# Performance work log

Measured on AMD Instinct MI355X. Metric: run time of the kernel, lower is better.

Reference implementation:

```python
import jax, jax.numpy as jnp
import numpy as np

N, IN_DIM, UNITS, Z_DEPTH, Z_K = 8192, 1024, 512, 32, 256


def setup_inputs() -> dict:
    key = jax.random.key(0)
    ks = jax.random.split(key, 10)
    s = 0.02
    return {
        "x": jax.random.normal(ks[0], (N, IN_DIM), jnp.float32),
        "h_W": jax.random.normal(ks[1], (IN_DIM, UNITS), jnp.float32) * s,
        "h_U": jax.random.normal(ks[2], (UNITS, UNITS), jnp.float32) * s,
        "h_b": jnp.zeros((UNITS,), jnp.float32),
        "f_W": jax.random.normal(ks[3], (UNITS, UNITS), jnp.float32) * s,
        "f_b": jnp.zeros((UNITS,), jnp.float32),
        "i_W": jax.random.normal(ks[4], (UNITS, UNITS), jnp.float32) * s,
        "i_b": jnp.zeros((UNITS,), jnp.float32),
        "c_W": jax.random.normal(ks[5], (UNITS, UNITS), jnp.float32) * s,
        "c_b": jnp.zeros((UNITS,), jnp.float32),
        "o_W": jax.random.normal(ks[6], (UNITS, UNITS), jnp.float32) * s,
        "o_b": jnp.zeros((UNITS,), jnp.float32),
        "t_W": jax.random.normal(ks[7], (UNITS, UNITS), jnp.float32) * s,
        "t_b": jnp.zeros((UNITS,), jnp.float32),
        "y_W": jax.random.normal(ks[8], (UNITS, Z_K), jnp.float32) * s,
        "y_b": jnp.zeros((Z_K,), jnp.float32),
        "h0": jnp.zeros((1, UNITS), jnp.float32),
        "z_depth": Z_DEPTH,
    }


def reference(x, h_W, h_U, h_b, f_W, f_b, i_W, i_b, c_W, c_b, o_W, o_b,
              t_W, t_b, y_W, y_b, h0, z_depth):
    n = x.shape[0]
    # x @ h_W is the same every step; hoist it out of the scan.
    xh = x @ h_W + h_b  # [n, units]

    def step(h_prev, _):
        h = jnp.tanh(xh + h_prev @ h_U)
        f = jax.nn.sigmoid(h @ f_W + f_b)
        i = jax.nn.sigmoid(h @ i_W + i_b)
        c = jnp.tanh(h @ c_W + c_b)
        o = jax.nn.sigmoid(h @ o_W + o_b)
        h1 = h_prev * f + c * i
        t = jnp.tanh((o * h1) @ t_W + t_b)
        y = jnp.tanh(t @ y_W + y_b)  # activation=tanh
        return h1, y

    h_init = jnp.broadcast_to(h0, (n, h0.shape[1]))
    _, ys = jax.lax.scan(step, h_init, None, length=z_depth)  # ys: [z_depth, n, z_k]
    return jnp.transpose(ys, (1, 0, 2))  # [n, z_depth, z_k]
```

## Files before the change

### kernel.cpp

```cpp
#include <hip/hip_runtime.h>


typedef _Float16 half_t;
typedef _Float16 half8 __attribute__((ext_vector_type(8)));
typedef _Float16 half4v __attribute__((ext_vector_type(4)));
typedef float float4_ __attribute__((ext_vector_type(4)));

#define UNITS 512
#define IN_DIM 1024
#define NROWS 8192
#define DEPTH 32
#define ZK 256
#define MT 64
#define PITCH (UNITS + 8)
#define XPITCH (IN_DIM + 8)

__device__ inline float4_ mfma16(half8 a, half8 b, float4_ c) {
  return __builtin_amdgcn_mfma_f32_16x16x32_f16(a, b, c, 0, 0, 0);
}
__device__ inline float fast_sigmoid(float x) {
  return __builtin_amdgcn_rcpf(1.0f + __builtin_amdgcn_exp2f(-1.4426950408889634f * x));
}
__device__ inline float fast_tanh(float x) {
  return 2.0f * __builtin_amdgcn_rcpf(1.0f + __builtin_amdgcn_exp2f(-2.8853900817779268f * x)) - 1.0f;
}

template<int NM, class OffF>
__device__ inline void sweepW(const half_t* __restrict__ wbase, OffF off,
                              const half_t* __restrict__ abase,
                              float4_ (&acc)[NM][4]) {
#pragma unroll
  for (int i = 0; i < NM; ++i)
#pragma unroll
    for (int rb = 0; rb < 4; ++rb) acc[i][rb] = {0.f, 0.f, 0.f, 0.f};
  for (int k0 = 0; k0 < UNITS; k0 += 64) {
    half8 a0[4], a1[4];
#pragma unroll
    for (int rb = 0; rb < 4; ++rb) {
      a0[rb] = *(const half8*)(abase + rb * 16 * PITCH + k0);
      a1[rb] = *(const half8*)(abase + rb * 16 * PITCH + k0 + 32);
    }
#pragma unroll
    for (int i = 0; i < NM; ++i) {
      const half_t* wp = wbase + off(i) + k0;
      half8 w0 = *(const half8*)(wp);
      half8 w1 = *(const half8*)(wp + 32);
#pragma unroll
      for (int rb = 0; rb < 4; ++rb) {
        acc[i][rb] = mfma16(w0, a0[rb], acc[i][rb]);
        acc[i][rb] = mfma16(w1, a1[rb], acc[i][rb]);
      }
    }
  }
}

template<int NB, int K, int AP, class OffF>
__device__ inline void stage_gemm(const half_t* __restrict__ bbase, OffF off,
                                  const half_t* __restrict__ A, int q, int c16,
                                  float4_ (&acc)[NB][2]) {
#pragma unroll
  for (int nb = 0; nb < NB; ++nb) {
    acc[nb][0] = {0.f, 0.f, 0.f, 0.f};
    acc[nb][1] = {0.f, 0.f, 0.f, 0.f};
  }
  for (int k0 = 0; k0 < K; k0 += 64) {
    const half_t* ap = A + c16 * AP + k0 + q * 8;
    half8 a00 = *(const half8*)(ap);
    half8 a01 = *(const half8*)(ap + 32);
    half8 a10 = *(const half8*)(ap + 16 * AP);
    half8 a11 = *(const half8*)(ap + 16 * AP + 32);
#pragma unroll
    for (int nb = 0; nb < NB; ++nb) {
      const half_t* bp = bbase + off(nb) + k0;
      half8 b0 = *(const half8*)(bp);
      half8 b1 = *(const half8*)(bp + 32);
      acc[nb][0] = mfma16(a00, b0, acc[nb][0]);
      acc[nb][0] = mfma16(a01, b1, acc[nb][0]);
      acc[nb][1] = mfma16(a10, b0, acc[nb][1]);
      acc[nb][1] = mfma16(a11, b1, acc[nb][1]);
    }
  }
}

__global__ void transpose_convert(const float* __restrict__ in, half_t* __restrict__ out,
                                  int R, int C) {
  __shared__ float tile[32][33];
  int c0 = blockIdx.x * 32, r0 = blockIdx.y * 32;
  int tx = threadIdx.x, ty = threadIdx.y;
#pragma unroll
  for (int i = 0; i < 32; i += 8)
    tile[ty + i][tx] = in[(size_t)(r0 + ty + i) * C + c0 + tx];
  __syncthreads();
#pragma unroll
  for (int i = 0; i < 32; i += 8)
    out[(size_t)(c0 + ty + i) * R + r0 + tx] = (half_t)tile[tx][ty + i];
}

__global__ __launch_bounds__(512, 2) void xh_kernel(
    const float* __restrict__ x, const half_t* __restrict__ hW_T,
    const float* __restrict__ h_b, half_t* __restrict__ xh_g) {
  extern __shared__ half_t sx[];
  const int tid = threadIdx.x;
  const int w = tid >> 6, l = tid & 63, q = l >> 4, c16 = l & 15;
  const int row0 = blockIdx.x * 32;
  for (int it = tid; it < 32 * IN_DIM / 4; it += 512) {
    int r = it >> 8;
    int c = (it & 255) * 4;
    float4_ v = __builtin_nontemporal_load((const float4_*)(x + (size_t)(row0 + r) * IN_DIM + c));
    half4v hv;
    hv[0] = (half_t)v[0]; hv[1] = (half_t)v[1]; hv[2] = (half_t)v[2]; hv[3] = (half_t)v[3];
    *(half4v*)(sx + r * XPITCH + c) = hv;
  }
  __syncthreads();
  const int n0 = w * 64;
  float4_ acc[4][2];
  const half_t* bbase = hW_T + (size_t)(n0 + c16) * IN_DIM + q * 8;
  stage_gemm<4, IN_DIM, XPITCH>(bbase, [](int nb) { return nb * 16 * IN_DIM; }, sx, q, c16, acc);
#pragma unroll
  for (int nb = 0; nb < 4; ++nb)
#pragma unroll
    for (int mb = 0; mb < 2; ++mb)
#pragma unroll
      for (int r = 0; r < 4; ++r) {
        int row = mb * 16 + q * 4 + r;
        int col = n0 + nb * 16 + c16;
        xh_g[(size_t)(row0 + row) * UNITS + col] = (half_t)(acc[nb][mb][r] + h_b[col]);
      }
}

__global__ __launch_bounds__(512, 2) void lstm_main(
    const half_t* __restrict__ xh_g, const half_t* __restrict__ hU_T,
    const half_t* __restrict__ W4_T, const half_t* __restrict__ tW_T,
    const half_t* __restrict__ yW_T,
    const float* __restrict__ f_b, const float* __restrict__ i_b,
    const float* __restrict__ c_b, const float* __restrict__ o_b,
    const float* __restrict__ t_b, const float* __restrict__ y_b,
    const float* __restrict__ h0, float* __restrict__ out) {
  extern __shared__ half_t smem[];
  half_t* bufA = smem;
  half_t* bufB = smem + MT * PITCH;

  const int tid = threadIdx.x;
  const int w = tid >> 6, l = tid & 63, q = l >> 4, c16 = l & 15;
  const int row0 = blockIdx.x * MT;

  for (int it = tid; it < MT * UNITS / 8; it += 512) {
    int r = it >> 6;
    int c = (it & 63) * 8;
    float4_ v0 = *(const float4_*)(h0 + c);
    float4_ v1 = *(const float4_*)(h0 + c + 4);
    half8 hv;
#pragma unroll
    for (int j = 0; j < 4; ++j) { hv[j] = (half_t)v0[j]; hv[4 + j] = (half_t)v1[j]; }
    *(half8*)(bufA + r * PITCH + c) = hv;
  }
  half4v state_r[2][2][4];
#pragma unroll
  for (int hh = 0; hh < 2; ++hh)
#pragma unroll
    for (int cm = 0; cm < 2; ++cm) {
      int col0 = hh * 256 + w * 32 + cm * 16 + q * 4;
      float4_ v = *(const float4_*)(h0 + col0);
      half4v s4;
#pragma unroll
      for (int r = 0; r < 4; ++r) s4[r] = (half_t)v[r];
#pragma unroll
      for (int rb = 0; rb < 4; ++rb) state_r[hh][cm][rb] = s4;
    }
  __syncthreads();

  for (int s = 0; s < DEPTH; ++s) {
    {
      float4_ acc[4][4];
      const half_t* wb = hU_T + (size_t)(w * 64 + c16) * UNITS + q * 8;
      sweepW<4>(wb, [](int i) { return i * 16 * UNITS; }, bufA + c16 * PITCH + q * 8, acc);
#pragma unroll
      for (int cm = 0; cm < 4; ++cm) {
        int col0 = w * 64 + cm * 16 + q * 4;
#pragma unroll
        for (int rb = 0; rb < 4; ++rb) {
          int row = rb * 16 + c16;
          half4v xh4 = *(const half4v*)(xh_g + (size_t)(row0 + row) * UNITS + col0);
          half4v hv;
#pragma unroll
          for (int r = 0; r < 4; ++r) hv[r] = (half_t)fast_tanh(acc[cm][rb][r] + (float)xh4[r]);
          *(half4v*)(bufB + row * PITCH + col0) = hv;
        }
      }
    }
    __syncthreads();
#pragma unroll 1
    for (int hh = 0; hh < 2; ++hh) {
      float4_ acc[8][4];
      const int colbase = hh * 256 + w * 32;
      const half_t* wb = W4_T + (size_t)(colbase + c16) * UNITS + q * 8;
      sweepW<8>(wb, [](int i) { return (i >> 1) * (UNITS * UNITS) + (i & 1) * 16 * UNITS; },
                bufB + c16 * PITCH + q * 8, acc);
#pragma unroll
      for (int cm = 0; cm < 2; ++cm) {
        int col0 = colbase + cm * 16 + q * 4;
        float4_ fb4 = *(const float4_*)(f_b + col0);
        float4_ ib4 = *(const float4_*)(i_b + col0);
        float4_ cb4 = *(const float4_*)(c_b + col0);
        float4_ ob4 = *(const float4_*)(o_b + col0);
#pragma unroll
        for (int rb = 0; rb < 4; ++rb) {
          int row = rb * 16 + c16;
          half4v hp = state_r[hh][cm][rb];
          half4v h1v, sbv;
#pragma unroll
          for (int r = 0; r < 4; ++r) {
            float gf = fast_sigmoid(acc[0 * 2 + cm][rb][r] + fb4[r]);
            float gi = fast_sigmoid(acc[1 * 2 + cm][rb][r] + ib4[r]);
            float gc = fast_tanh   (acc[2 * 2 + cm][rb][r] + cb4[r]);
            float go = fast_sigmoid(acc[3 * 2 + cm][rb][r] + ob4[r]);
            float h1 = (float)hp[r] * gf + gc * gi;
            h1v[r] = (half_t)h1;
            sbv[r] = (half_t)(go * h1);
          }
          state_r[hh][cm][rb] = h1v;
          *(half4v*)(bufA + row * PITCH + col0) = sbv;
        }
      }
    }
    __syncthreads();
    {
      float4_ acc[4][4];
      const half_t* wb = tW_T + (size_t)(w * 64 + c16) * UNITS + q * 8;
      sweepW<4>(wb, [](int i) { return i * 16 * UNITS; }, bufA + c16 * PITCH + q * 8, acc);
#pragma unroll
      for (int cm = 0; cm < 4; ++cm) {
        int col0 = w * 64 + cm * 16 + q * 4;
        float4_ tb4 = *(const float4_*)(t_b + col0);
#pragma unroll
        for (int rb = 0; rb < 4; ++rb) {
          int row = rb * 16 + c16;
          half4v hv;
#pragma unroll
          for (int r = 0; r < 4; ++r) hv[r] = (half_t)fast_tanh(acc[cm][rb][r] + tb4[r]);
          *(half4v*)(bufB + row * PITCH + col0) = hv;
        }
      }
    }
    __syncthreads();
    {
      float4_ acc[2][4];
      const half_t* wb = yW_T + (size_t)(w * 32 + c16) * UNITS + q * 8;
      sweepW<2>(wb, [](int i) { return i * 16 * UNITS; }, bufB + c16 * PITCH + q * 8, acc);
#pragma unroll
      for (int cm = 0; cm < 2; ++cm) {
        int col0 = w * 32 + cm * 16 + q * 4;
        float4_ yb4 = *(const float4_*)(y_b + col0);
#pragma unroll
        for (int rb = 0; rb < 4; ++rb) {
          int row = rb * 16 + c16;
          float4_ yv;
#pragma unroll
          for (int r = 0; r < 4; ++r) yv[r] = fast_tanh(acc[cm][rb][r] + yb4[r]);
          __builtin_nontemporal_store(yv,
              (float4_*)(out + ((size_t)(row0 + row) * DEPTH + s) * ZK + col0));
        }
      }
#pragma unroll
      for (int hh = 0; hh < 2; ++hh)
#pragma unroll
        for (int cm = 0; cm < 2; ++cm) {
          int col0 = hh * 256 + w * 32 + cm * 16 + q * 4;
#pragma unroll
          for (int rb = 0; rb < 4; ++rb)
            *(half4v*)(bufA + (rb * 16 + c16) * PITCH + col0) = state_r[hh][cm][rb];
        }
    }
    __syncthreads();
  }
}

extern "C" void kernel_launch(void* const* d_in, const int* in_sizes, int n_in,
                              void* d_out, int out_size, void* d_ws, size_t ws_size,
                              hipStream_t stream) {
  (void)in_sizes; (void)n_in; (void)out_size; (void)ws_size;
  const float* x   = (const float*)d_in[0];
  const float* h_W = (const float*)d_in[1];
  const float* h_U = (const float*)d_in[2];
  const float* h_b = (const float*)d_in[3];
  const float* f_W = (const float*)d_in[4];
  const float* f_b = (const float*)d_in[5];
  const float* i_W = (const float*)d_in[6];
  const float* i_b = (const float*)d_in[7];
  const float* c_W = (const float*)d_in[8];
  const float* c_b = (const float*)d_in[9];
  const float* o_W = (const float*)d_in[10];
  const float* o_b = (const float*)d_in[11];
  const float* t_W = (const float*)d_in[12];
  const float* t_b = (const float*)d_in[13];
  const float* y_W = (const float*)d_in[14];
  const float* y_b = (const float*)d_in[15];
  const float* h0  = (const float*)d_in[16];
  float* out = (float*)d_out;

  half_t* ws   = (half_t*)d_ws;
  half_t* hW_T = ws;
  half_t* hU_T = hW_T + (size_t)UNITS * IN_DIM;
  half_t* W4_T = hU_T + (size_t)UNITS * UNITS;
  half_t* tW_T = W4_T + (size_t)4 * UNITS * UNITS;
  half_t* yW_T = tW_T + (size_t)UNITS * UNITS;
  half_t* xh_g = yW_T + (size_t)ZK * UNITS;

  hipFuncSetAttribute((const void*)xh_kernel, hipFuncAttributeMaxDynamicSharedMemorySize,
                      32 * XPITCH * 2);
  hipFuncSetAttribute((const void*)lstm_main, hipFuncAttributeMaxDynamicSharedMemorySize,
                      2 * MT * PITCH * 2);

  dim3 tb(32, 8);
  hipLaunchKernelGGL(transpose_convert, dim3(UNITS / 32, IN_DIM / 32), tb, 0, stream,
                     h_W, hW_T, IN_DIM, UNITS);
  hipLaunchKernelGGL(transpose_convert, dim3(UNITS / 32, UNITS / 32), tb, 0, stream,
                     h_U, hU_T, UNITS, UNITS);
  hipLaunchKernelGGL(transpose_convert, dim3(UNITS / 32, UNITS / 32), tb, 0, stream,
                     f_W, W4_T + 0 * (size_t)UNITS * UNITS, UNITS, UNITS);
  hipLaunchKernelGGL(transpose_convert, dim3(UNITS / 32, UNITS / 32), tb, 0, stream,
                     i_W, W4_T + 1 * (size_t)UNITS * UNITS, UNITS, UNITS);
  hipLaunchKernelGGL(transpose_convert, dim3(UNITS / 32, UNITS / 32), tb, 0, stream,
                     c_W, W4_T + 2 * (size_t)UNITS * UNITS, UNITS, UNITS);
  hipLaunchKernelGGL(transpose_convert, dim3(UNITS / 32, UNITS / 32), tb, 0, stream,
                     o_W, W4_T + 3 * (size_t)UNITS * UNITS, UNITS, UNITS);
  hipLaunchKernelGGL(transpose_convert, dim3(UNITS / 32, UNITS / 32), tb, 0, stream,
                     t_W, tW_T, UNITS, UNITS);
  hipLaunchKernelGGL(transpose_convert, dim3(ZK / 32, UNITS / 32), tb, 0, stream,
                     y_W, yW_T, UNITS, ZK);
  hipLaunchKernelGGL(xh_kernel, dim3(NROWS / 32), dim3(512), 32 * XPITCH * 2, stream,
                     x, hW_T, h_b, xh_g);
  hipLaunchKernelGGL(lstm_main, dim3(NROWS / MT), dim3(512), 2 * MT * PITCH * 2, stream,
                     xh_g, hU_T, W4_T, tW_T, yW_T, f_b, i_b, c_b, o_b, t_b, y_b, h0, out);
}
```

Measured before the change: 4.401 ms.

## Halve row tile, double-buffer weight loads, stage xh and biases in LDS

```diff
diff --git a/kernel.cpp b/kernel.cpp
--- a/kernel.cpp
+++ b/kernel.cpp
@@ -11,7 +11,7 @@
 #define NROWS 8192
 #define DEPTH 32
 #define ZK 256
-#define MT 64
+#define MT 32
 #define PITCH (UNITS + 8)
 #define XPITCH (IN_DIM + 8)
 
@@ -28,28 +28,38 @@
 template<int NM, class OffF>
 __device__ inline void sweepW(const half_t* __restrict__ wbase, OffF off,
                               const half_t* __restrict__ abase,
-                              float4_ (&acc)[NM][4]) {
-#pragma unroll
-  for (int i = 0; i < NM; ++i)
-#pragma unroll
-    for (int rb = 0; rb < 4; ++rb) acc[i][rb] = {0.f, 0.f, 0.f, 0.f};
-  for (int k0 = 0; k0 < UNITS; k0 += 64) {
-    half8 a0[4], a1[4];
-#pragma unroll
-    for (int rb = 0; rb < 4; ++rb) {
-      a0[rb] = *(const half8*)(abase + rb * 16 * PITCH + k0);
-      a1[rb] = *(const half8*)(abase + rb * 16 * PITCH + k0 + 32);
-    }
+                              float4_ (&acc)[NM][2]) {
+#pragma unroll
+  for (int i = 0; i < NM; ++i) {
+    acc[i][0] = {0.f, 0.f, 0.f, 0.f};
+    acc[i][1] = {0.f, 0.f, 0.f, 0.f};
+  }
+  half8 w0[2][NM], w1[2][NM];
+#pragma unroll
+  for (int i = 0; i < NM; ++i) {
+    w0[0][i] = *(const half8*)(wbase + off(i));
+    w1[0][i] = *(const half8*)(wbase + off(i) + 32);
+  }
+#pragma unroll
+  for (int kk = 0; kk < 8; ++kk) {
+    const int cur = kk & 1, nxt = cur ^ 1;
+    const int knext = ((kk + 1) & 7) * 64;
 #pragma unroll
     for (int i = 0; i < NM; ++i) {
-      const half_t* wp = wbase + off(i) + k0;
-      half8 w0 = *(const half8*)(wp);
-      half8 w1 = *(const half8*)(wp + 32);
-#pragma unroll
-      for (int rb = 0; rb < 4; ++rb) {
-        acc[i][rb] = mfma16(w0, a0[rb], acc[i][rb]);
-        acc[i][rb] = mfma16(w1, a1[rb], acc[i][rb]);
-      }
+      w0[nxt][i] = *(const half8*)(wbase + off(i) + knext);
+      w1[nxt][i] = *(const half8*)(wbase + off(i) + knext + 32);
+    }
+    const int k0 = kk * 64;
+    half8 a00 = *(const half8*)(abase + k0);
+    half8 a01 = *(const half8*)(abase + k0 + 32);
+    half8 a10 = *(const half8*)(abase + 16 * PITCH + k0);
+    half8 a11 = *(const half8*)(abase + 16 * PITCH + k0 + 32);
+#pragma unroll
+    for (int i = 0; i < NM; ++i) {
+      acc[i][0] = mfma16(w0[cur][i], a00, acc[i][0]);
+      acc[i][0] = mfma16(w1[cur][i], a01, acc[i][0]);
+      acc[i][1] = mfma16(w0[cur][i], a10, acc[i][1]);
+      acc[i][1] = mfma16(w1[cur][i], a11, acc[i][1]);
     }
   }
 }
@@ -139,6 +149,14 @@
   extern __shared__ half_t smem[];
   half_t* bufA = smem;
   half_t* bufB = smem + MT * PITCH;
+  half_t* s_xh = smem + 2 * MT * PITCH;
+  float* s_bias = (float*)(smem + 3 * MT * PITCH);
+  float* s_fb = s_bias;
+  float* s_ib = s_bias + 512;
+  float* s_cb = s_bias + 1024;
+  float* s_ob = s_bias + 1536;
+  float* s_tb = s_bias + 2048;
+  float* s_yb = s_bias + 2560;
 
   const int tid = threadIdx.x;
   const int w = tid >> 6, l = tid & 63, q = l >> 4, c16 = l & 15;
@@ -153,8 +171,14 @@
 #pragma unroll
     for (int j = 0; j < 4; ++j) { hv[j] = (half_t)v0[j]; hv[4 + j] = (half_t)v1[j]; }
     *(half8*)(bufA + r * PITCH + c) = hv;
-  }
-  half4v state_r[2][2][4];
+    *(half8*)(s_xh + r * PITCH + c) = *(const half8*)(xh_g + (size_t)(row0 + r) * UNITS + c);
+  }
+  for (int it = tid; it < 512; it += 512) {
+    s_fb[it] = f_b[it]; s_ib[it] = i_b[it]; s_cb[it] = c_b[it]; s_ob[it] = o_b[it];
+    s_tb[it] = t_b[it];
+    if (it < 256) s_yb[it] = y_b[it];
+  }
+  half4v state_r[2][2][2];
 #pragma unroll
   for (int hh = 0; hh < 2; ++hh)
 #pragma unroll
@@ -165,22 +189,25 @@
 #pragma unroll
       for (int r = 0; r < 4; ++r) s4[r] = (half_t)v[r];
 #pragma unroll
-      for (int rb = 0; rb < 4; ++rb) state_r[hh][cm][rb] = s4;
+      for (int rb = 0; rb < 2; ++rb) state_r[hh][cm][rb] = s4;
     }
   __syncthreads();
+
+  const half_t* abase_off = (const half_t*)0 + c16 * PITCH + q * 8;
+  (void)abase_off;
 
   for (int s = 0; s < DEPTH; ++s) {
     {
-      float4_ acc[4][4];
+      float4_ acc[4][2];
       const half_t* wb = hU_T + (size_t)(w * 64 + c16) * UNITS + q * 8;
       sweepW<4>(wb, [](int i) { return i * 16 * UNITS; }, bufA + c16 * PITCH + q * 8, acc);
 #pragma unroll
       for (int cm = 0; cm < 4; ++cm) {
         int col0 = w * 64 + cm * 16 + q * 4;
 #pragma unroll
-        for (int rb = 0; rb < 4; ++rb) {
+        for (int rb = 0; rb < 2; ++rb) {
           int row = rb * 16 + c16;
-          half4v xh4 = *(const half4v*)(xh_g + (size_t)(row0 + row) * UNITS + col0);
+          half4v xh4 = *(const half4v*)(s_xh + row * PITCH + col0);
           half4v hv;
 #pragma unroll
           for (int r = 0; r < 4; ++r) hv[r] = (half_t)fast_tanh(acc[cm][rb][r] + (float)xh4[r]);
@@ -191,7 +218,7 @@
     __syncthreads();
 #pragma unroll 1
     for (int hh = 0; hh < 2; ++hh) {
-      float4_ acc[8][4];
+      float4_ acc[8][2];
       const int colbase = hh * 256 + w * 32;
       const half_t* wb = W4_T + (size_t)(colbase + c16) * UNITS + q * 8;
       sweepW<8>(wb, [](int i) { return (i >> 1) * (UNITS * UNITS) + (i & 1) * 16 * UNITS; },
@@ -199,12 +226,12 @@
 #pragma unroll
       for (int cm = 0; cm < 2; ++cm) {
         int col0 = colbase + cm * 16 + q * 4;
-        float4_ fb4 = *(const float4_*)(f_b + col0);
-        float4_ ib4 = *(const float4_*)(i_b + col0);
-        float4_ cb4 = *(const float4_*)(c_b + col0);
-        float4_ ob4 = *(const float4_*)(o_b + col0);
-#pragma unroll
-        for (int rb = 0; rb < 4; ++rb) {
+        float4_ fb4 = *(const float4_*)(s_fb + col0);
+        float4_ ib4 = *(const float4_*)(s_ib + col0);
+        float4_ cb4 = *(const float4_*)(s_cb + col0);
+        float4_ ob4 = *(const float4_*)(s_ob + col0);
+#pragma unroll
+        for (int rb = 0; rb < 2; ++rb) {
           int row = rb * 16 + c16;
           half4v hp = state_r[hh][cm][rb];
           half4v h1v, sbv;
@@ -225,15 +252,15 @@
     }
     __syncthreads();
     {
-      float4_ acc[4][4];
+      float4_ acc[4][2];
       const half_t* wb = tW_T + (size_t)(w * 64 + c16) * UNITS + q * 8;
       sweepW<4>(wb, [](int i) { return i * 16 * UNITS; }, bufA + c16 * PITCH + q * 8, acc);
 #pragma unroll
       for (int cm = 0; cm < 4; ++cm) {
         int col0 = w * 64 + cm * 16 + q * 4;
-        float4_ tb4 = *(const float4_*)(t_b + col0);
-#pragma unroll
-        for (int rb = 0; rb < 4; ++rb) {
+        float4_ tb4 = *(const float4_*)(s_tb + col0);
+#pragma unroll
+        for (int rb = 0; rb < 2; ++rb) {
           int row = rb * 16 + c16;
           half4v hv;
 #pragma unroll
@@ -244,15 +271,15 @@
     }
     __syncthreads();
     {
-      float4_ acc[2][4];
+      float4_ acc[2][2];
       const half_t* wb = yW_T + (size_t)(w * 32 + c16) * UNITS + q * 8;
       sweepW<2>(wb, [](int i) { return i * 16 * UNITS; }, bufB + c16 * PITCH + q * 8, acc);
 #pragma unroll
       for (int cm = 0; cm < 2; ++cm) {
         int col0 = w * 32 + cm * 16 + q * 4;
-        float4_ yb4 = *(const float4_*)(y_b + col0);
-#pragma unroll
-        for (int rb = 0; rb < 4; ++rb) {
+        float4_ yb4 = *(const float4_*)(s_yb + col0);
+#pragma unroll
+        for (int rb = 0; rb < 2; ++rb) {
           int row = rb * 16 + c16;
           float4_ yv;
 #pragma unroll
@@ -267,7 +294,7 @@
         for (int cm = 0; cm < 2; ++cm) {
           int col0 = hh * 256 + w * 32 + cm * 16 + q * 4;
 #pragma unroll
-          for (int rb = 0; rb < 4; ++rb)
+          for (int rb = 0; rb < 2; ++rb)
             *(half4v*)(bufA + (rb * 16 + c16) * PITCH + col0) = state_r[hh][cm][rb];
         }
     }
@@ -306,10 +333,11 @@
   half_t* yW_T = tW_T + (size_t)UNITS * UNITS;
   half_t* xh_g = yW_T + (size_t)ZK * UNITS;
 
+  const int lds_main = 3 * MT * PITCH * 2 + 2816 * 4;
   hipFuncSetAttribute((const void*)xh_kernel, hipFuncAttributeMaxDynamicSharedMemorySize,
                       32 * XPITCH * 2);
   hipFuncSetAttribute((const void*)lstm_main, hipFuncAttributeMaxDynamicSharedMemorySize,
-                      2 * MT * PITCH * 2);
+                      lds_main);
 
   dim3 tb(32, 8);
   hipLaunchKernelGGL(transpose_convert, dim3(UNITS / 32, IN_DIM / 32), tb, 0, stream,
@@ -330,6 +358,6 @@
                      y_W, yW_T, UNITS, ZK);
   hipLaunchKernelGGL(xh_kernel, dim3(NROWS / 32), dim3(512), 32 * XPITCH * 2, stream,
                      x, hW_T, h_b, xh_g);
-  hipLaunchKernelGGL(lstm_main, dim3(NROWS / MT), dim3(512), 2 * MT * PITCH * 2, stream,
+  hipLaunchKernelGGL(lstm_main, dim3(NROWS / MT), dim3(512), lds_main, stream,
                      xh_g, hU_T, W4_T, tW_T, yW_T, f_b, i_b, c_b, o_b, t_b, y_b, h0, out);
 }
```

After: 4.360 ms. No clear change (-0.9%).
